# Optimization experiments

Measured on AMD Instinct MI355X. Metric: run time of the kernel, lower is better.

## Reference

```python
import math
import jax, jax.numpy as jnp
import numpy as np

C = 1.0          # Poincare ball curvature
NUM_HEADS = 8
EPS = 1e-15

def _beta(a, b):
    # Beta function via lgamma (python float constant)
    return math.exp(math.lgamma(a) + math.lgamma(b) - math.lgamma(a + b))

def h_linear(x, z, r, c=C):
    """HNN++ Poincare fully-connected layer (hypll HLinear).
    x: [..., in] points in the ball; z: [in, out] tangent weights; r: [out] bias."""
    sc = math.sqrt(c)
    x2 = jnp.sum(x * x, axis=-1, keepdims=True)
    lam = 2.0 / (1.0 - c * x2)                                # conformal factor
    zn = jnp.maximum(jnp.linalg.norm(z, axis=0), EPS)          # [out]
    inner = x @ z                                              # [..., out]
    two_scr = 2.0 * sc * r
    d = (2.0 * zn / sc) * jnp.arcsinh(
        (sc * inner * lam / zn) * jnp.cosh(two_scr) - (lam - 1.0) * jnp.sinh(two_scr)
    )
    w = jnp.sinh(sc * d) / sc
    return w / (1.0 + jnp.sqrt(1.0 + c * jnp.sum(w * w, axis=-1, keepdims=True)))

def pairwise_dist(q, k, c=C):
    """Poincare distance d(q,k) = arccosh(1 + 2c|q-k|^2 / ((1-c|q|^2)(1-c|k|^2))) / sqrt(c).
    q,k: [B,H,S,hd] -> [B,H,S,S]."""
    q2 = jnp.sum(q * q, axis=-1)
    k2 = jnp.sum(k * k, axis=-1)
    qk = jnp.einsum('bhqd,bhkd->bhqk', q, k)
    diff2 = jnp.maximum(q2[..., :, None] + k2[..., None, :] - 2.0 * qk, 0.0)
    denom = (1.0 - c * q2)[..., :, None] * (1.0 - c * k2)[..., None, :]
    arg = 1.0 + 2.0 * c * diff2 / denom
    return jnp.arccosh(jnp.maximum(arg, 1.0 + 1e-7)) / math.sqrt(c)

def midpoint(v, w, c=C):
    """Weighted Mobius gyromidpoint: m = 1/2 (x) (sum w*lam*x / sum w*(lam-1)).
    v: [B,H,Sk,hd], w: [B,H,Sq,Sk] -> [B,H,Sq,hd]."""
    v2 = jnp.sum(v * v, axis=-1)                      # [B,H,Sk]
    lam = 2.0 / (1.0 - c * v2)
    num = jnp.einsum('bhqk,bhkd->bhqd', w * lam[..., None, :], v)
    den = jnp.maximum(jnp.einsum('bhqk,bhk->bhq', w, lam - 1.0), EPS)[..., None]
    g = num / den                                     # gyromidpoint pre-scaling
    sc = math.sqrt(c)
    gn = jnp.maximum(jnp.linalg.norm(g, axis=-1, keepdims=True), EPS)
    t = jnp.tanh(0.5 * jnp.arctanh(jnp.clip(sc * gn, 0.0, 1.0 - 1e-7)))
    return (t / sc) * g / gn

def _forward(query, key, value, Wq, bq, Wk, bk, Wv, bv, scale_tau, scale_gamma):
    B, S, E = query.shape
    H = NUM_HEADS
    hd = E // H
    # hyperbolic q/k/v projections, then split into heads: [B,H,S,hd]
    q = h_linear(query, Wq, bq).reshape(B, S, H, hd).transpose(0, 2, 1, 3)
    k = h_linear(key, Wk, bk).reshape(B, S, H, hd).transpose(0, 2, 1, 3)
    v = h_linear(value, Wv, bv).reshape(B, S, H, hd).transpose(0, 2, 1, 3)
    # similarity = -dist/tau - gamma with tau = exp(-scale_tau)
    sim = -pairwise_dist(q, k) * jnp.exp(scale_tau[0]) - scale_gamma[0]
    causal = jnp.triu(jnp.ones((S, S), dtype=bool), k=1)
    sim = jnp.where(causal, -jnp.inf, sim)
    w = jnp.exp(sim)                                  # 'exp' attention activation
    agg = midpoint(v, w)                              # [B,H,S,hd]
    agg = agg.transpose(0, 2, 1, 3).reshape(B, S, E)
    # HNN++ beta-concatenation of the per-head ball points
    scale = _beta(E / 2.0, 0.5) / _beta(hd / 2.0, 0.5)
    return agg * scale

def setup_inputs() -> dict:
    root = jax.random.key(0)
    ks = jax.random.split(root, 8)
    B, S, E = 1, 2048, 512
    s = 0.02  # keep points well inside the unit ball
    return {
        'query': s * jax.random.normal(ks[0], (B, S, E), jnp.float32),
        'key':   s * jax.random.normal(ks[1], (B, S, E), jnp.float32),
        'value': s * jax.random.normal(ks[2], (B, S, E), jnp.float32),
        'Wq': s * jax.random.normal(ks[3], (E, E), jnp.float32),
        'Wk': s * jax.random.normal(ks[4], (E, E), jnp.float32),
        'Wv': s * jax.random.normal(ks[5], (E, E), jnp.float32),
        'bq': jnp.zeros((E,), jnp.float32),
        'bk': jnp.zeros((E,), jnp.float32),
        'bv': jnp.zeros((E,), jnp.float32),
        'scale_tau': jnp.zeros((1,), jnp.float32),
        'scale_gamma': jnp.zeros((1,), jnp.float32),
    }

def reference(query, key, value, Wq, Wk, Wv, bq, bk, bv, scale_tau, scale_gamma):
    return _forward(query, key, value, Wq, bq, Wk, bk, Wv, bv, scale_tau, scale_gamma)
```

## Files before the change

kernel.cpp:

```cpp
#include <hip/hip_runtime.h>
#include <cmath>

#define H 8
#define SEQ 2048
#define EDIM 512
#define HD 64
#define EPSF 1e-15f

typedef short bf16x8 __attribute__((ext_vector_type(8)));
typedef float f32x4 __attribute__((ext_vector_type(4)));

#define ZN_OFF    16
#define STATS_OFF (ZN_OFF + 24 * EDIM)
#define CQ_OFF    (STATS_OFF + 3 * H * SEQ)
#define IK_OFF    (CQ_OFF + H * SEQ)
#define PX2_OFF   (IK_OFF + H * SEQ)
#define U16_OFF   (PX2_OFF + 12288 + 16)
#define WT_U16    0
#define QKVB_U16  (WT_U16 + 3 * EDIM * EDIM)
#define VT_U16    (QKVB_U16 + 3 * SEQ * EDIM)
#define U16_TOTAL (VT_U16 + H * 80 * SEQ)
#define BIG_OFF   (U16_OFF + U16_TOTAL / 2 + 16)
#define TRI16 2112
#define PART_U16S (H * TRI16 * 1280)
#define ACC_FLOATS  (H * SEQ * 80)

__device__ __forceinline__ float bf2f(unsigned short u){
  union { unsigned int i; float f; } v; v.i = ((unsigned int)u) << 16; return v.f;
}
__device__ __forceinline__ unsigned short f2bf(float f){
  union { float f; unsigned int i; } v; v.f = f;
  unsigned int x = v.i;
  unsigned int r = (x + 0x7fffu + ((x >> 16) & 1u)) >> 16;
  return (unsigned short)r;
}

__device__ __forceinline__ unsigned int cvt_pk_bf16(float a, float b){
  unsigned int r;
  asm("v_cvt_pk_bf16_f32 %0, %1, %2" : "=v"(r) : "v"(a), "v"(b));
  return r;
}
__device__ __forceinline__ float vlog2f(float x){
  float r; asm("v_log_f32 %0, %1" : "=v"(r) : "v"(x)); return r;
}
__device__ __forceinline__ float vexp2f(float x){
  float r; asm("v_exp_f32 %0, %1" : "=v"(r) : "v"(x)); return r;
}
__device__ __forceinline__ float vsqrtf(float x){
  float r; asm("v_sqrt_f32 %0, %1" : "=v"(r) : "v"(x)); return r;
}

__device__ __forceinline__ int detect_f32(const unsigned short* __restrict__ q){
  const int l = threadIdx.x & 63;
  float mx = 0.f;
  #pragma unroll
  for (int j = 0; j < 4; ++j) mx = fmaxf(mx, fabsf(bf2f(q[l * 4 + j])));
  #pragma unroll
  for (int m = 32; m >= 1; m >>= 1) mx = fmaxf(mx, __shfl_xor(mx, m, 64));
  return mx > 1000.f;
}

__device__ __forceinline__ int sbase(int s){
  const int a = s >> 2, b = s & 3;
  return s + 2 * a * (a - 1) + a * b;
}

__global__ __launch_bounds__(256) void wcvt_kernel(
    const void* __restrict__ Wq, const void* __restrict__ Wk, const void* __restrict__ Wv,
    const unsigned short* __restrict__ qprobe,
    unsigned short* __restrict__ WT, float* __restrict__ zn)
{
  const int p = blockIdx.y;
  const int bi = blockIdx.x >> 3, bo = blockIdx.x & 7;
  const void* W = (p == 0) ? Wq : ((p == 1) ? Wk : Wv);
  const int t = threadIdx.x;
  const int isf32 = detect_f32(qprobe);
  __shared__ float tile[64][65];

  #pragma unroll
  for (int j = 0; j < 16; ++j){
    int idx = t + 256 * j;
    int il = idx >> 6, ol = idx & 63;
    float val;
    if (isf32) val = ((const float*)W)[(size_t)(bi * 64 + il) * EDIM + bo * 64 + ol];
    else       val = bf2f(((const unsigned short*)W)[(size_t)(bi * 64 + il) * EDIM + bo * 64 + ol]);
    tile[il][ol] = val;
  }
  __syncthreads();
  if (t < 64){
    float s = 0.f;
    #pragma unroll 8
    for (int i = 0; i < 64; ++i){ float v = tile[i][t]; s += v * v; }
    zn[((size_t)(bi * 3 + p)) * EDIM + bo * 64 + t] = s;
  }
  #pragma unroll
  for (int j = 0; j < 16; ++j){
    int idx = t + 256 * j;
    int ol = idx >> 6, il = idx & 63;
    WT[((size_t)p * EDIM + bo * 64 + ol) * EDIM + bi * 64 + il] = f2bf(tile[il][ol]);
  }
}

__global__ __launch_bounds__(256) void hlin_gemm_kernel(
    const void* __restrict__ Xq, const void* __restrict__ Xk, const void* __restrict__ Xv,
    const unsigned short* __restrict__ WT, const unsigned short* __restrict__ qprobe,
    unsigned short* __restrict__ partC, float* __restrict__ partX2)
{
  const int p = blockIdx.y;
  const int rg = blockIdx.x >> 1;
  const int kslice = blockIdx.x & 1;
  const void* X = (p == 0) ? Xq : ((p == 1) ? Xk : Xv);
  const int r0 = rg * 16;
  const int t  = threadIdx.x;
  const int w = t >> 6, lane = t & 63;
  const int col = lane & 15, quad = lane >> 4;
  const int isf32 = detect_f32(qprobe);
  const int koff = kslice * 256;

  const unsigned short* WTb = WT + ((size_t)p * EDIM + w * 128 + col) * EDIM + koff;
  const float* Xf = (const float*)X + (size_t)(r0 + col) * EDIM + koff;
  const unsigned short* Xh = (const unsigned short*)X + (size_t)(r0 + col) * EDIM + koff;

  f32x4 acc[8];
  #pragma unroll
  for (int nt = 0; nt < 8; ++nt) acc[nt] = (f32x4){0.f, 0.f, 0.f, 0.f};
  float x2part = 0.f;

  bf16x8 caf, naf;
  bf16x8 cbf[8], nbf[8];
  {
    if (isf32){
      float4 xa = *(const float4*)&Xf[quad * 8];
      float4 xb = *(const float4*)&Xf[quad * 8 + 4];
      float xv[8] = {xa.x, xa.y, xa.z, xa.w, xb.x, xb.y, xb.z, xb.w};
      #pragma unroll
      for (int j = 0; j < 8; ++j){ caf[j] = (short)f2bf(xv[j]); x2part += xv[j] * xv[j]; }
    } else {
      caf = *(const bf16x8*)&Xh[quad * 8];
      #pragma unroll
      for (int j = 0; j < 8; ++j){ float xv = bf2f((unsigned short)caf[j]); x2part += xv * xv; }
    }
    #pragma unroll
    for (int nt = 0; nt < 8; ++nt)
      cbf[nt] = *(const bf16x8*)&WTb[(size_t)nt * 16 * EDIM + quad * 8];
  }

  for (int ks = 0; ks < 8; ++ks){
    if (ks + 1 < 8){
      const int off = (ks + 1) * 32 + quad * 8;
      if (isf32){
        float4 xa = *(const float4*)&Xf[off];
        float4 xb = *(const float4*)&Xf[off + 4];
        float xv[8] = {xa.x, xa.y, xa.z, xa.w, xb.x, xb.y, xb.z, xb.w};
        #pragma unroll
        for (int j = 0; j < 8; ++j){ naf[j] = (short)f2bf(xv[j]); x2part += xv[j] * xv[j]; }
      } else {
        naf = *(const bf16x8*)&Xh[off];
        #pragma unroll
        for (int j = 0; j < 8; ++j){ float xv = bf2f((unsigned short)naf[j]); x2part += xv * xv; }
      }
      #pragma unroll
      for (int nt = 0; nt < 8; ++nt)
        nbf[nt] = *(const bf16x8*)&WTb[(size_t)nt * 16 * EDIM + off];
    }
    #pragma unroll
    for (int nt = 0; nt < 8; ++nt)
      acc[nt] = __builtin_amdgcn_mfma_f32_16x16x32_bf16(caf, cbf[nt], acc[nt], 0, 0, 0);
    if (ks + 1 < 8){
      caf = naf;
      #pragma unroll
      for (int nt = 0; nt < 8; ++nt) cbf[nt] = nbf[nt];
    }
  }
  x2part += __shfl_xor(x2part, 16, 64);
  x2part += __shfl_xor(x2part, 32, 64);

  const size_t base = ((size_t)(p * 128 + rg) * 2 + kslice) * 8192;
  #pragma unroll
  for (int nt = 0; nt < 8; ++nt)
    #pragma unroll
    for (int r = 0; r < 4; ++r)
      partC[base + (size_t)(quad * 4 + r) * 512 + w * 128 + nt * 16 + col] = f2bf(acc[nt][r]);
  if (w == 0 && quad == 0)
    partX2[((size_t)(p * 128 + rg) * 2 + kslice) * 16 + col] = x2part;
}

__global__ __launch_bounds__(256) void hlin_fin_kernel(
    const unsigned short* __restrict__ partC, const float* __restrict__ partX2,
    const void* __restrict__ Bq, const void* __restrict__ Bk, const void* __restrict__ Bv,
    const float* __restrict__ znacc, const unsigned short* __restrict__ qprobe,
    unsigned short* __restrict__ qkvb, float* __restrict__ stats,
    float* __restrict__ cqs, float* __restrict__ iks,
    unsigned short* __restrict__ VT)
{
  const int p = blockIdx.y;
  const void* Bb = (p == 0) ? Bq : ((p == 1) ? Bk : Bv);
  const int rg = blockIdx.x;
  const int r0 = rg * 16;
  const int t  = threadIdx.x;
  const int w = t >> 6, lane = t & 63;
  const int col = lane & 15, quad = lane >> 4;
  const int isf32 = detect_f32(qprobe);

  __shared__ float smem[16 * EDIM];
  __shared__ float sw2[16];

  const size_t base0 = ((size_t)(p * 128 + rg) * 2 + 0) * 8192;
  const size_t base1 = base0 + 8192;

  f32x4 acc[8];
  #pragma unroll
  for (int nt = 0; nt < 8; ++nt)
    #pragma unroll
    for (int r = 0; r < 4; ++r){
      const size_t idx = (size_t)(quad * 4 + r) * 512 + w * 128 + nt * 16 + col;
      acc[nt][r] = bf2f(partC[base0 + idx]) + bf2f(partC[base1 + idx]);
    }

  float lamr[4], lm1[4];
  #pragma unroll
  for (int r = 0; r < 4; ++r){
    const int row = quad * 4 + r;
    float x2r = partX2[((size_t)(p * 128 + rg) * 2 + 0) * 16 + row] +
                partX2[((size_t)(p * 128 + rg) * 2 + 1) * 16 + row];
    lamr[r] = 2.f / (1.f - x2r);
    lm1[r] = lamr[r] - 1.f;
  }
  #pragma unroll
  for (int nt = 0; nt < 8; ++nt){
    const int n = w * 128 + nt * 16 + col;
    float zsum = 0.f;
    #pragma unroll
    for (int bi = 0; bi < 8; ++bi)
      zsum += znacc[((size_t)(bi * 3 + p)) * EDIM + n];
    float znv = fmaxf(sqrtf(zsum), EPSF);
    float rb;
    if (isf32) rb = ((const float*)Bb)[n];
    else       rb = bf2f(((const unsigned short*)Bb)[n]);
    float e2r = __expf(2.f * rb);
    float ie2r = 1.f / e2r;
    float ch = 0.5f * (e2r + ie2r), sh = 0.5f * (e2r - ie2r);
    float izn = 1.f / znv;
    float tz = 2.f * znv;
    #pragma unroll
    for (int r = 0; r < 4; ++r){
      float a = (acc[nt][r] * lamr[r] * izn) * ch - lm1[r] * sh;
      float b = a + sqrtf(a * a + 1.f);
      float tt = __expf(tz * __logf(b));
      smem[(quad * 4 + r) * EDIM + n] = 0.5f * (tt - 1.f / tt);
    }
  }
  __syncthreads();

  {
    int row = t >> 4, l = t & 15;
    float s = 0.f;
    for (int o = l; o < EDIM; o += 16){ float wv = smem[row * EDIM + o]; s += wv * wv; }
    #pragma unroll
    for (int m = 8; m >= 1; m >>= 1) s += __shfl_xor(s, m, 16);
    if (l == 0) sw2[row] = s;
  }
  __syncthreads();

  const int o0 = 2 * t;
  const int h0 = t >> 5;
  const int d0 = o0 & 63;
  const int l5 = t & 31;
  #pragma unroll
  for (int rr = 0; rr < 16; ++rr){
    float inv = 1.f / (1.f + sqrtf(1.f + sw2[rr]));
    unsigned short b0 = f2bf(smem[rr * EDIM + o0] * inv);
    unsigned short b1 = f2bf(smem[rr * EDIM + o0 + 1] * inv);
    float r0v = bf2f(b0), r1v = bf2f(b1);
    int s = r0 + rr;
    unsigned int* dst = (unsigned int*)&qkvb[(((size_t)p * H + h0) * SEQ + s) * HD + d0];
    *dst = (unsigned int)b0 | ((unsigned int)b1 << 16);
    float ss = r0v * r0v + r1v * r1v;
    #pragma unroll
    for (int m = 16; m >= 1; m >>= 1) ss += __shfl_xor(ss, m, 64);
    if (p == 2){
      float lam = 2.f / (1.f - ss);
      VT[((size_t)h0 * 80 + d0) * SEQ + s]     = f2bf(r0v * lam);
      VT[((size_t)h0 * 80 + d0 + 1) * SEQ + s] = f2bf(r1v * lam);
      if (l5 < 16)
        VT[((size_t)h0 * 80 + 64 + l5) * SEQ + s] = (l5 == 0) ? f2bf(lam - 1.f) : 0;
    }
    if (l5 == 0){
      stats[((size_t)p * H + h0) * SEQ + s] = ss;
      if (p == 0) cqs[(size_t)h0 * SEQ + s] = 2.f / (1.f - ss);
      if (p == 1) iks[(size_t)h0 * SEQ + s] = 1.f / (1.f - ss);
    }
  }
}

__device__ __forceinline__ uint4 xpose32(unsigned int tlo0, unsigned int tlo1,
                                         unsigned int thi0, unsigned int thi1,
                                         int srcA, int srcB, int tsel){
  unsigned int a0 = (unsigned int)__shfl((int)tlo0, srcA, 64);
  unsigned int a1 = (unsigned int)__shfl((int)tlo1, srcA, 64);
  unsigned int b0 = (unsigned int)__shfl((int)thi0, srcA, 64);
  unsigned int b1 = (unsigned int)__shfl((int)thi1, srcA, 64);
  unsigned int c0 = (unsigned int)__shfl((int)tlo0, srcB, 64);
  unsigned int c1 = (unsigned int)__shfl((int)tlo1, srcB, 64);
  unsigned int d0 = (unsigned int)__shfl((int)thi0, srcB, 64);
  unsigned int d1 = (unsigned int)__shfl((int)thi1, srcB, 64);
  uint4 r;
  r.x = tsel ? a1 : a0;
  r.y = tsel ? b1 : b0;
  r.z = tsel ? c1 : c0;
  r.w = tsel ? d1 : d0;
  return r;
}

__device__ __forceinline__ void score4(
    const f32x4& s4, const float4& k2v, const float4& ikv,
    float cq, float cqq2, float m2cq, int kbase, int qmax, int quad,
    float m_et, float m_g2, unsigned int& lo, unsigned int& hi)
{
  float w[4];
  #pragma unroll
  for (int r = 0; r < 4; ++r){
    float k2 = (r == 0) ? k2v.x : (r == 1) ? k2v.y : (r == 2) ? k2v.z : k2v.w;
    float ik = (r == 0) ? ikv.x : (r == 1) ? ikv.y : (r == 2) ? ikv.z : ikv.w;
    float t1 = __builtin_fmaf(k2, cq, cqq2);
    t1 = __builtin_fmaf(m2cq, s4[r], t1);
    float u = fmaxf(t1 * ik, 1e-7f);
    float z = 1.f + u + vsqrtf(u * (u + 2.f));
    float wv = vexp2f(__builtin_fmaf(vlog2f(z), m_et, m_g2));
    const int key = kbase + quad * 4 + r;
    w[r] = (key > qmax) ? 0.f : wv;
  }
  lo = cvt_pk_bf16(w[0], w[1]);
  hi = cvt_pk_bf16(w[2], w[3]);
}

template<int NITER>
__device__ __forceinline__ void attn_qloop(
    int s0, int c, int kBeg, int col, int quad, int lane,
    const unsigned short* __restrict__ Qh,
    const bf16x8 (&kf0)[4], const bf16x8 (&kf1)[4],
    const float4 (&ck2)[4], const float4 (&cik)[4],
    const bf16x8 (&vf0)[5], const bf16x8 (&vf1)[5],
    const float* __restrict__ q2s, const float* __restrict__ cqs,
    float m_et, float m_g2, int srcA, int srcB, int tsel,
    float* __restrict__ big, int h, int use_part)
{
  bf16x8 qA0 = *(const bf16x8*)&Qh[(size_t)(s0 * 16 + col) * HD + quad * 8];
  bf16x8 qA1 = *(const bf16x8*)&Qh[(size_t)(s0 * 16 + col) * HD + 32 + quad * 8];
  bf16x8 qB0 = *(const bf16x8*)&Qh[(size_t)((s0 + 1) * 16 + col) * HD + quad * 8];
  bf16x8 qB1 = *(const bf16x8*)&Qh[(size_t)((s0 + 1) * 16 + col) * HD + 32 + quad * 8];
  float q2A = q2s[s0 * 16 + col],       cqA = cqs[s0 * 16 + col];
  float q2B = q2s[(s0 + 1) * 16 + col], cqB = cqs[(s0 + 1) * 16 + col];

  #pragma unroll
  for (int i = 0; i < NITER; ++i){
    const int sA = s0 + 2 * i, sB = sA + 1;
    bf16x8 nA0, nA1, nB0, nB1;
    float nq2A, ncqA, nq2B, ncqB;
    if (i + 1 < NITER){
      const int tA = (sA + 2) * 16 + col, tB = (sA + 3) * 16 + col;
      nA0 = *(const bf16x8*)&Qh[(size_t)tA * HD + quad * 8];
      nA1 = *(const bf16x8*)&Qh[(size_t)tA * HD + 32 + quad * 8];
      nB0 = *(const bf16x8*)&Qh[(size_t)tB * HD + quad * 8];
      nB1 = *(const bf16x8*)&Qh[(size_t)tB * HD + 32 + quad * 8];
      nq2A = q2s[tA]; ncqA = cqs[tA];
      nq2B = q2s[tB]; ncqB = cqs[tB];
    }

    const float cqq2A = cqA * q2A, m2cqA = -2.f * cqA;
    const float cqq2B = cqB * q2B, m2cqB = -2.f * cqB;
    const int qmaxA = sA * 16 + col, qmaxB = sB * 16 + col;

    f32x4 sSA[4], sSB[4];
    __builtin_amdgcn_s_setprio(1);
    #pragma unroll
    for (int g = 0; g < 4; ++g){
      f32x4 z4 = (f32x4){0.f, 0.f, 0.f, 0.f};
      sSA[g] = __builtin_amdgcn_mfma_f32_16x16x32_bf16(kf0[g], qA0, z4, 0, 0, 0);
      sSA[g] = __builtin_amdgcn_mfma_f32_16x16x32_bf16(kf1[g], qA1, sSA[g], 0, 0, 0);
      sSB[g] = __builtin_amdgcn_mfma_f32_16x16x32_bf16(kf0[g], qB0, z4, 0, 0, 0);
      sSB[g] = __builtin_amdgcn_mfma_f32_16x16x32_bf16(kf1[g], qB1, sSB[g], 0, 0, 0);
    }
    __builtin_amdgcn_s_setprio(0);

    unsigned int loA[4], hiA[4], loB[4], hiB[4];
    #pragma unroll
    for (int g = 0; g < 4; ++g){
      score4(sSA[g], ck2[g], cik[g], cqA, cqq2A, m2cqA, kBeg + g * 16, qmaxA, quad,
             m_et, m_g2, loA[g], hiA[g]);
      score4(sSB[g], ck2[g], cik[g], cqB, cqq2B, m2cqB, kBeg + g * 16, qmaxB, quad,
             m_et, m_g2, loB[g], hiB[g]);
    }

    union { uint4 u; bf16x8 v; } pA01, pA23, pB01, pB23;
    pA01.u = xpose32(loA[0], loA[1], hiA[0], hiA[1], srcA, srcB, tsel);
    pA23.u = xpose32(loA[2], loA[3], hiA[2], hiA[3], srcA, srcB, tsel);
    pB01.u = xpose32(loB[0], loB[1], hiB[0], hiB[1], srcA, srcB, tsel);
    pB23.u = xpose32(loB[2], loB[3], hiB[2], hiB[3], srcA, srcB, tsel);

    f32x4 pvA[5], pvB[5];
    __builtin_amdgcn_s_setprio(1);
    #pragma unroll
    for (int nt = 0; nt < 5; ++nt){
      f32x4 z4 = (f32x4){0.f, 0.f, 0.f, 0.f};
      pvA[nt] = __builtin_amdgcn_mfma_f32_16x16x32_bf16(pA01.v, vf0[nt], z4, 0, 0, 0);
      pvA[nt] = __builtin_amdgcn_mfma_f32_16x16x32_bf16(pA23.v, vf1[nt], pvA[nt], 0, 0, 0);
      pvB[nt] = __builtin_amdgcn_mfma_f32_16x16x32_bf16(pB01.v, vf0[nt], z4, 0, 0, 0);
      pvB[nt] = __builtin_amdgcn_mfma_f32_16x16x32_bf16(pB23.v, vf1[nt], pvB[nt], 0, 0, 0);
    }
    __builtin_amdgcn_s_setprio(0);

    if (use_part){
      uint2* slotA = (uint2*)big + (size_t)(h * TRI16 + sbase(sA) + c) * 320;
      uint2* slotB = (uint2*)big + (size_t)(h * TRI16 + sbase(sB) + c) * 320;
      #pragma unroll
      for (int nt = 0; nt < 5; ++nt){
        uint2 pk;
        pk.x = cvt_pk_bf16(pvA[nt][0], pvA[nt][1]);
        pk.y = cvt_pk_bf16(pvA[nt][2], pvA[nt][3]);
        slotA[nt * 64 + lane] = pk;
        pk.x = cvt_pk_bf16(pvB[nt][0], pvB[nt][1]);
        pk.y = cvt_pk_bf16(pvB[nt][2], pvB[nt][3]);
        slotB[nt * 64 + lane] = pk;
      }
    } else {
      #pragma unroll
      for (int r = 0; r < 4; ++r){
        float* rowA = big + ((size_t)h * SEQ + sA * 16 + quad * 4 + r) * 80;
        float* rowB = big + ((size_t)h * SEQ + sB * 16 + quad * 4 + r) * 80;
        #pragma unroll
        for (int nt = 0; nt < 5; ++nt){
          atomicAdd(&rowA[16 * nt + col], pvA[nt][r]);
          atomicAdd(&rowB[16 * nt + col], pvB[nt][r]);
        }
      }
    }

    if (i + 1 < NITER){
      qA0 = nA0; qA1 = nA1; qB0 = nB0; qB1 = nB1;
      q2A = nq2A; cqA = ncqA; q2B = nq2B; cqB = ncqB;
    }
  }
}

__global__ __launch_bounds__(64, 2) void attn_kernel(
    const unsigned short* __restrict__ Qb, const unsigned short* __restrict__ Kb,
    const unsigned short* __restrict__ VT,
    const float* __restrict__ q2s_all, const float* __restrict__ k2s_all,
    const float* __restrict__ cqs_all, const float* __restrict__ iks_all,
    const void* __restrict__ tau, const void* __restrict__ gam,
    const unsigned short* __restrict__ qprobe,
    float* __restrict__ big, int use_part)
{
  const int h = blockIdx.y;
  const int c = blockIdx.x >> 4;
  const int j = blockIdx.x & 15;
  const int nsl = (33 - c) >> 1;
  if (j >= nsl) return;
  const int kBeg = c * 64;
  const int s0 = 4 * c + 8 * j;
  const int rem = 128 - s0;
  const int lane = threadIdx.x;
  const int col = lane & 15, quad = lane >> 4;

  const unsigned short* Qh  = Qb + (size_t)h * SEQ * HD;
  const unsigned short* Kh  = Kb + (size_t)h * SEQ * HD;
  const unsigned short* VTh = VT + (size_t)h * 80 * SEQ;
  const float* q2s = q2s_all + (size_t)h * SEQ;
  const float* k2s = k2s_all + (size_t)h * SEQ;
  const float* cqs = cqs_all + (size_t)h * SEQ;
  const float* iks = iks_all + (size_t)h * SEQ;

  const int isf32 = detect_f32(qprobe);
  float tauv, gamv;
  if (isf32){ tauv = ((const float*)tau)[0]; gamv = ((const float*)gam)[0]; }
  else      { tauv = bf2f(((const unsigned short*)tau)[0]);
              gamv = bf2f(((const unsigned short*)gam)[0]); }
  const float m_et = -__expf(tauv);
  const float m_g2 = -gamv * 1.44269504088896340736f;

  const int srcA = ((quad & 1) * 2) * 16 + col;
  const int srcB = srcA + 16;
  const int tsel = quad >> 1;

  bf16x8 kf0[4], kf1[4];
  float4 ck2[4], cik[4];
  #pragma unroll
  for (int g = 0; g < 4; ++g){
    kf0[g] = *(const bf16x8*)&Kh[(size_t)(kBeg + g * 16 + col) * HD + quad * 8];
    kf1[g] = *(const bf16x8*)&Kh[(size_t)(kBeg + g * 16 + col) * HD + 32 + quad * 8];
    ck2[g] = *(const float4*)&k2s[kBeg + g * 16 + quad * 4];
    cik[g] = *(const float4*)&iks[kBeg + g * 16 + quad * 4];
  }
  bf16x8 vf0[5], vf1[5];
  #pragma unroll
  for (int nt = 0; nt < 5; ++nt){
    vf0[nt] = *(const bf16x8*)&VTh[(size_t)(16 * nt + col) * SEQ + kBeg + quad * 8];
    vf1[nt] = *(const bf16x8*)&VTh[(size_t)(16 * nt + col) * SEQ + kBeg + 32 + quad * 8];
  }

  if (rem >= 8)
    attn_qloop<4>(s0, c, kBeg, col, quad, lane, Qh, kf0, kf1, ck2, cik, vf0, vf1,
                  q2s, cqs, m_et, m_g2, srcA, srcB, tsel, big, h, use_part);
  else
    attn_qloop<2>(s0, c, kBeg, col, quad, lane, Qh, kf0, kf1, ck2, cik, vf0, vf1,
                  q2s, cqs, m_et, m_g2, srcA, srcB, tsel, big, h, use_part);
}

__global__ __launch_bounds__(256) void attn_fin_kernel(
    const float* __restrict__ big, int use_part,
    float* __restrict__ out, float beta_scale)
{
  const int h = blockIdx.y, s = blockIdx.x;
  const int t = threadIdx.x;
  const int w = t >> 6, lane = t & 63;
  const int col = lane & 15, quad = lane >> 4;
  const int q0 = s * 16;

  __shared__ float red[4][64][20];

  f32x4 pv[5];
  #pragma unroll
  for (int nt = 0; nt < 5; ++nt) pv[nt] = (f32x4){0.f, 0.f, 0.f, 0.f};

  if (use_part){
    const int tbase = sbase(s);
    const int nv = (s >> 2) + 1;
    for (int sl = w; sl < nv; sl += 4){
      const uint2* slot = (const uint2*)big + (size_t)(h * TRI16 + tbase + sl) * 320;
      #pragma unroll
      for (int nt = 0; nt < 5; ++nt){
        uint2 v = slot[nt * 64 + lane];
        pv[nt][0] += bf2f((unsigned short)(v.x & 0xffffu));
        pv[nt][1] += bf2f((unsigned short)(v.x >> 16));
        pv[nt][2] += bf2f((unsigned short)(v.y & 0xffffu));
        pv[nt][3] += bf2f((unsigned short)(v.y >> 16));
      }
    }
  } else if (w == 0){
    #pragma unroll
    for (int nt = 0; nt < 5; ++nt)
      #pragma unroll
      for (int r = 0; r < 4; ++r)
        pv[nt][r] = big[((size_t)h * SEQ + q0 + quad * 4 + r) * 80 + 16 * nt + col];
  }

  #pragma unroll
  for (int nt = 0; nt < 5; ++nt)
    *(float4*)&red[w][lane][nt * 4] = (float4){pv[nt][0], pv[nt][1], pv[nt][2], pv[nt][3]};
  __syncthreads();

  if (t < 64){
    #pragma unroll
    for (int nt = 0; nt < 5; ++nt){
      float4 a = *(const float4*)&red[0][t][nt * 4];
      float4 b = *(const float4*)&red[1][t][nt * 4];
      float4 c = *(const float4*)&red[2][t][nt * 4];
      float4 d = *(const float4*)&red[3][t][nt * 4];
      pv[nt][0] = a.x + b.x + c.x + d.x;
      pv[nt][1] = a.y + b.y + c.y + d.y;
      pv[nt][2] = a.z + b.z + c.z + d.z;
      pv[nt][3] = a.w + b.w + c.w + d.w;
    }
    #pragma unroll
    for (int r = 0; r < 4; ++r){
      float den = __shfl(pv[4][r], quad * 16, 64);
      den = fmaxf(den, EPSF);
      float inv_den = 1.f / den;
      float g[4];
      float gsq = 0.f;
      #pragma unroll
      for (int nt = 0; nt < 4; ++nt){ g[nt] = pv[nt][r] * inv_den; gsq += g[nt] * g[nt]; }
      #pragma unroll
      for (int m = 8; m >= 1; m >>= 1) gsq += __shfl_xor(gsq, m, 64);
      float gn = fmaxf(sqrtf(gsq), EPSF);
      float x = fminf(gn, 1.f - 1e-7f);
      float tt2 = x / (1.f + sqrtf(1.f - x * x));
      float scl = (tt2 / gn) * beta_scale;
      const int q = q0 + quad * 4 + r;
      #pragma unroll
      for (int nt = 0; nt < 4; ++nt)
        out[(size_t)q * EDIM + h * HD + 16 * nt + col] = g[nt] * scl;
    }
  }
}

extern "C" void kernel_launch(void* const* d_in, const int* in_sizes, int n_in,
                              void* d_out, int out_size, void* d_ws, size_t ws_size,
                              hipStream_t stream){
  const void* Xq  = d_in[0];
  const void* Xk  = d_in[1];
  const void* Xv  = d_in[2];
  const void* Wq  = d_in[3];
  const void* Wk  = d_in[4];
  const void* Wv  = d_in[5];
  const void* Bq  = d_in[6];
  const void* Bk  = d_in[7];
  const void* Bv  = d_in[8];
  const void* tau = d_in[9];
  const void* gam = d_in[10];

  float* wsf   = (float*)d_ws;
  float* zn    = wsf + ZN_OFF;
  float* stats = wsf + STATS_OFF;
  float* cqs   = wsf + CQ_OFF;
  float* iks   = wsf + IK_OFF;
  float* px2   = wsf + PX2_OFF;
  unsigned short* u16b = (unsigned short*)(wsf + U16_OFF);
  unsigned short* WT   = u16b + WT_U16;
  unsigned short* qkvb = u16b + QKVB_U16;
  unsigned short* VT   = u16b + VT_U16;
  float* big   = wsf + BIG_OFF;
  unsigned short* partC = (unsigned short*)big;

  const int use_part =
      (ws_size >= (size_t)BIG_OFF * sizeof(float) + (size_t)PART_U16S * 2) ? 1 : 0;

  unsigned short* Qb = qkvb;
  unsigned short* Kb = qkvb + (size_t)H * SEQ * HD;
  float* q2s = stats;
  float* k2s = stats + (size_t)H * SEQ;
  const unsigned short* qprobe = (const unsigned short*)Xq;

  double lb1 = lgamma(EDIM / 2.0) + lgamma(0.5) - lgamma(EDIM / 2.0 + 0.5);
  double lb2 = lgamma(HD / 2.0)   + lgamma(0.5) - lgamma(HD / 2.0 + 0.5);
  float beta_scale = (float)exp(lb1 - lb2);

  wcvt_kernel<<<dim3(64, 3), dim3(256), 0, stream>>>(Wq, Wk, Wv, qprobe, WT, zn);
  hlin_gemm_kernel<<<dim3(256, 3), dim3(256), 0, stream>>>(
      Xq, Xk, Xv, WT, qprobe, partC, px2);
  hlin_fin_kernel<<<dim3(128, 3), dim3(256), 0, stream>>>(
      partC, px2, Bq, Bk, Bv, zn, qprobe, qkvb, stats, cqs, iks, VT);
  if (!use_part)
    hipMemsetAsync(big, 0, (size_t)ACC_FLOATS * sizeof(float), stream);
  attn_kernel<<<dim3(512, H), dim3(64), 0, stream>>>(
      Qb, Kb, VT, q2s, k2s, cqs, iks, tau, gam, qprobe, big, use_part);
  attn_fin_kernel<<<dim3(128, H), dim3(256), 0, stream>>>(
      big, use_part, (float*)d_out, beta_scale);
}
```

Before: 186.4 us.

## Split attention work into smaller per-block query slices with upfront Q loads

The attention kernel now gives each block 4 query tiles instead of 8, which doubles the grid to 1024 blocks per head. The templated query loop with rolling Q prefetch is removed. All four Q tiles and their stats are now loaded into registers at the start. This aims to improve load balance and occupancy over the triangular causal work. In exchange it reloads the K/V fragments for twice as many blocks and writes more partial results or atomics, and it holds more live registers per thread.

```diff
diff --git a/kernel.cpp b/kernel.cpp
--- a/kernel.cpp
+++ b/kernel.cpp
@@ -334,41 +334,76 @@
   hi = cvt_pk_bf16(w[2], w[3]);
 }
 
-template<int NITER>
-__device__ __forceinline__ void attn_qloop(
-    int s0, int c, int kBeg, int col, int quad, int lane,
-    const unsigned short* __restrict__ Qh,
-    const bf16x8 (&kf0)[4], const bf16x8 (&kf1)[4],
-    const float4 (&ck2)[4], const float4 (&cik)[4],
-    const bf16x8 (&vf0)[5], const bf16x8 (&vf1)[5],
-    const float* __restrict__ q2s, const float* __restrict__ cqs,
-    float m_et, float m_g2, int srcA, int srcB, int tsel,
-    float* __restrict__ big, int h, int use_part)
+__global__ __launch_bounds__(64, 2) void attn_kernel(
+    const unsigned short* __restrict__ Qb, const unsigned short* __restrict__ Kb,
+    const unsigned short* __restrict__ VT,
+    const float* __restrict__ q2s_all, const float* __restrict__ k2s_all,
+    const float* __restrict__ cqs_all, const float* __restrict__ iks_all,
+    const void* __restrict__ tau, const void* __restrict__ gam,
+    const unsigned short* __restrict__ qprobe,
+    float* __restrict__ big, int use_part)
 {
-  bf16x8 qA0 = *(const bf16x8*)&Qh[(size_t)(s0 * 16 + col) * HD + quad * 8];
-  bf16x8 qA1 = *(const bf16x8*)&Qh[(size_t)(s0 * 16 + col) * HD + 32 + quad * 8];
-  bf16x8 qB0 = *(const bf16x8*)&Qh[(size_t)((s0 + 1) * 16 + col) * HD + quad * 8];
-  bf16x8 qB1 = *(const bf16x8*)&Qh[(size_t)((s0 + 1) * 16 + col) * HD + 32 + quad * 8];
-  float q2A = q2s[s0 * 16 + col],       cqA = cqs[s0 * 16 + col];
-  float q2B = q2s[(s0 + 1) * 16 + col], cqB = cqs[(s0 + 1) * 16 + col];
-
-  #pragma unroll
-  for (int i = 0; i < NITER; ++i){
-    const int sA = s0 + 2 * i, sB = sA + 1;
-    bf16x8 nA0, nA1, nB0, nB1;
-    float nq2A, ncqA, nq2B, ncqB;
-    if (i + 1 < NITER){
-      const int tA = (sA + 2) * 16 + col, tB = (sA + 3) * 16 + col;
-      nA0 = *(const bf16x8*)&Qh[(size_t)tA * HD + quad * 8];
-      nA1 = *(const bf16x8*)&Qh[(size_t)tA * HD + 32 + quad * 8];
-      nB0 = *(const bf16x8*)&Qh[(size_t)tB * HD + quad * 8];
-      nB1 = *(const bf16x8*)&Qh[(size_t)tB * HD + 32 + quad * 8];
-      nq2A = q2s[tA]; ncqA = cqs[tA];
-      nq2B = q2s[tB]; ncqB = cqs[tB];
-    }
-
-    const float cqq2A = cqA * q2A, m2cqA = -2.f * cqA;
-    const float cqq2B = cqB * q2B, m2cqB = -2.f * cqB;
+  const int h = blockIdx.y;
+  const int c = blockIdx.x >> 5;
+  const int j = blockIdx.x & 31;
+  if (j >= 32 - c) return;
+  const int kBeg = c * 64;
+  const int s0 = 4 * c + 4 * j;
+  const int lane = threadIdx.x;
+  const int col = lane & 15, quad = lane >> 4;
+
+  const unsigned short* Qh  = Qb + (size_t)h * SEQ * HD;
+  const unsigned short* Kh  = Kb + (size_t)h * SEQ * HD;
+  const unsigned short* VTh = VT + (size_t)h * 80 * SEQ;
+  const float* q2s = q2s_all + (size_t)h * SEQ;
+  const float* k2s = k2s_all + (size_t)h * SEQ;
+  const float* cqs = cqs_all + (size_t)h * SEQ;
+  const float* iks = iks_all + (size_t)h * SEQ;
+
+  const int isf32 = detect_f32(qprobe);
+  float tauv, gamv;
+  if (isf32){ tauv = ((const float*)tau)[0]; gamv = ((const float*)gam)[0]; }
+  else      { tauv = bf2f(((const unsigned short*)tau)[0]);
+              gamv = bf2f(((const unsigned short*)gam)[0]); }
+  const float m_et = -__expf(tauv);
+  const float m_g2 = -gamv * 1.44269504088896340736f;
+
+  const int srcA = ((quad & 1) * 2) * 16 + col;
+  const int srcB = srcA + 16;
+  const int tsel = quad >> 1;
+
+  bf16x8 kf0[4], kf1[4];
+  float4 ck2[4], cik[4];
+  #pragma unroll
+  for (int g = 0; g < 4; ++g){
+    kf0[g] = *(const bf16x8*)&Kh[(size_t)(kBeg + g * 16 + col) * HD + quad * 8];
+    kf1[g] = *(const bf16x8*)&Kh[(size_t)(kBeg + g * 16 + col) * HD + 32 + quad * 8];
+    ck2[g] = *(const float4*)&k2s[kBeg + g * 16 + quad * 4];
+    cik[g] = *(const float4*)&iks[kBeg + g * 16 + quad * 4];
+  }
+  bf16x8 vf0[5], vf1[5];
+  #pragma unroll
+  for (int nt = 0; nt < 5; ++nt){
+    vf0[nt] = *(const bf16x8*)&VTh[(size_t)(16 * nt + col) * SEQ + kBeg + quad * 8];
+    vf1[nt] = *(const bf16x8*)&VTh[(size_t)(16 * nt + col) * SEQ + kBeg + 32 + quad * 8];
+  }
+  bf16x8 qf0[4], qf1[4];
+  float q2v[4], cqv[4];
+  #pragma unroll
+  for (int u = 0; u < 4; ++u){
+    const int row = (s0 + u) * 16 + col;
+    qf0[u] = *(const bf16x8*)&Qh[(size_t)row * HD + quad * 8];
+    qf1[u] = *(const bf16x8*)&Qh[(size_t)row * HD + 32 + quad * 8];
+    q2v[u] = q2s[row];
+    cqv[u] = cqs[row];
+  }
+
+  #pragma unroll
+  for (int i = 0; i < 2; ++i){
+    const int uA = 2 * i, uB = uA + 1;
+    const int sA = s0 + uA, sB = s0 + uB;
+    const float cqA = cqv[uA], cqq2A = cqv[uA] * q2v[uA], m2cqA = -2.f * cqv[uA];
+    const float cqB = cqv[uB], cqq2B = cqv[uB] * q2v[uB], m2cqB = -2.f * cqv[uB];
     const int qmaxA = sA * 16 + col, qmaxB = sB * 16 + col;
 
     f32x4 sSA[4], sSB[4];
@@ -376,10 +411,10 @@
     #pragma unroll
     for (int g = 0; g < 4; ++g){
       f32x4 z4 = (f32x4){0.f, 0.f, 0.f, 0.f};
-      sSA[g] = __builtin_amdgcn_mfma_f32_16x16x32_bf16(kf0[g], qA0, z4, 0, 0, 0);
-      sSA[g] = __builtin_amdgcn_mfma_f32_16x16x32_bf16(kf1[g], qA1, sSA[g], 0, 0, 0);
-      sSB[g] = __builtin_amdgcn_mfma_f32_16x16x32_bf16(kf0[g], qB0, z4, 0, 0, 0);
-      sSB[g] = __builtin_amdgcn_mfma_f32_16x16x32_bf16(kf1[g], qB1, sSB[g], 0, 0, 0);
+      sSA[g] = __builtin_amdgcn_mfma_f32_16x16x32_bf16(kf0[g], qf0[uA], z4, 0, 0, 0);
+      sSA[g] = __builtin_amdgcn_mfma_f32_16x16x32_bf16(kf1[g], qf1[uA], sSA[g], 0, 0, 0);
+      sSB[g] = __builtin_amdgcn_mfma_f32_16x16x32_bf16(kf0[g], qf0[uB], z4, 0, 0, 0);
+      sSB[g] = __builtin_amdgcn_mfma_f32_16x16x32_bf16(kf1[g], qf1[uB], sSB[g], 0, 0, 0);
     }
     __builtin_amdgcn_s_setprio(0);
 
@@ -435,76 +470,7 @@
         }
       }
     }
-
-    if (i + 1 < NITER){
-      qA0 = nA0; qA1 = nA1; qB0 = nB0; qB1 = nB1;
-      q2A = nq2A; cqA = ncqA; q2B = nq2B; cqB = ncqB;
-    }
-  }
-}
-
-__global__ __launch_bounds__(64, 2) void attn_kernel(
-    const unsigned short* __restrict__ Qb, const unsigned short* __restrict__ Kb,
-    const unsigned short* __restrict__ VT,
-    const float* __restrict__ q2s_all, const float* __restrict__ k2s_all,
-    const float* __restrict__ cqs_all, const float* __restrict__ iks_all,
-    const void* __restrict__ tau, const void* __restrict__ gam,
-    const unsigned short* __restrict__ qprobe,
-    float* __restrict__ big, int use_part)
-{
-  const int h = blockIdx.y;
-  const int c = blockIdx.x >> 4;
-  const int j = blockIdx.x & 15;
-  const int nsl = (33 - c) >> 1;
-  if (j >= nsl) return;
-  const int kBeg = c * 64;
-  const int s0 = 4 * c + 8 * j;
-  const int rem = 128 - s0;
-  const int lane = threadIdx.x;
-  const int col = lane & 15, quad = lane >> 4;
-
-  const unsigned short* Qh  = Qb + (size_t)h * SEQ * HD;
-  const unsigned short* Kh  = Kb + (size_t)h * SEQ * HD;
-  const unsigned short* VTh = VT + (size_t)h * 80 * SEQ;
-  const float* q2s = q2s_all + (size_t)h * SEQ;
-  const float* k2s = k2s_all + (size_t)h * SEQ;
-  const float* cqs = cqs_all + (size_t)h * SEQ;
-  const float* iks = iks_all + (size_t)h * SEQ;
-
-  const int isf32 = detect_f32(qprobe);
-  float tauv, gamv;
-  if (isf32){ tauv = ((const float*)tau)[0]; gamv = ((const float*)gam)[0]; }
-  else      { tauv = bf2f(((const unsigned short*)tau)[0]);
-              gamv = bf2f(((const unsigned short*)gam)[0]); }
-  const float m_et = -__expf(tauv);
-  const float m_g2 = -gamv * 1.44269504088896340736f;
-
-  const int srcA = ((quad & 1) * 2) * 16 + col;
-  const int srcB = srcA + 16;
-  const int tsel = quad >> 1;
-
-  bf16x8 kf0[4], kf1[4];
-  float4 ck2[4], cik[4];
-  #pragma unroll
-  for (int g = 0; g < 4; ++g){
-    kf0[g] = *(const bf16x8*)&Kh[(size_t)(kBeg + g * 16 + col) * HD + quad * 8];
-    kf1[g] = *(const bf16x8*)&Kh[(size_t)(kBeg + g * 16 + col) * HD + 32 + quad * 8];
-    ck2[g] = *(const float4*)&k2s[kBeg + g * 16 + quad * 4];
-    cik[g] = *(const float4*)&iks[kBeg + g * 16 + quad * 4];
-  }
-  bf16x8 vf0[5], vf1[5];
-  #pragma unroll
-  for (int nt = 0; nt < 5; ++nt){
-    vf0[nt] = *(const bf16x8*)&VTh[(size_t)(16 * nt + col) * SEQ + kBeg + quad * 8];
-    vf1[nt] = *(const bf16x8*)&VTh[(size_t)(16 * nt + col) * SEQ + kBeg + 32 + quad * 8];
-  }
-
-  if (rem >= 8)
-    attn_qloop<4>(s0, c, kBeg, col, quad, lane, Qh, kf0, kf1, ck2, cik, vf0, vf1,
-                  q2s, cqs, m_et, m_g2, srcA, srcB, tsel, big, h, use_part);
-  else
-    attn_qloop<2>(s0, c, kBeg, col, quad, lane, Qh, kf0, kf1, ck2, cik, vf0, vf1,
-                  q2s, cqs, m_et, m_g2, srcA, srcB, tsel, big, h, use_part);
+  }
 }
 
 __global__ __launch_bounds__(256) void attn_fin_kernel(
@@ -633,7 +599,7 @@
       partC, px2, Bq, Bk, Bv, zn, qprobe, qkvb, stats, cqs, iks, VT);
   if (!use_part)
     hipMemsetAsync(big, 0, (size_t)ACC_FLOATS * sizeof(float), stream);
-  attn_kernel<<<dim3(512, H), dim3(64), 0, stream>>>(
+  attn_kernel<<<dim3(1024, H), dim3(64), 0, stream>>>(
       Qb, Kb, VT, q2s, k2s, cqs, iks, tau, gam, qprobe, big, use_part);
   attn_fin_kernel<<<dim3(128, H), dim3(256), 0, stream>>>(
       big, use_part, (float*)d_out, beta_scale);
```

Result: slower. 194.2 us (+4.2%).
